# Kernel tuning notes

Hardware: AMD Instinct MI355X
Metric: run time of the kernel (lower is better)

Reference implementation:

```python
import jax, jax.numpy as jnp
import numpy as np


def _gather(feat, idx):
    # feat: [B, L, F], idx: [B, L, D] -> [B, L, D, F]  (per-molecule neighbor gather)
    return jax.vmap(lambda f, i: f[i])(feat, idx)


def setup_inputs() -> dict:
    key = jax.random.key(0)
    ks = jax.random.split(key, 16)
    B, L, D, F, FA, FB, R = 256, 128, 6, 200, 39, 10, 2
    s = 0.05
    return {
        "atom_list": jax.random.normal(ks[0], (B, L, FA), jnp.float32),
        "bond_list": jax.random.normal(ks[1], (B, L, FB), jnp.float32),
        "atom_degree": jax.random.randint(ks[2], (B, L, D), 0, L, jnp.int32),
        "bond_degree": jax.random.randint(ks[3], (B, L, D), 0, L, jnp.int32),
        "atom_W": jax.random.normal(ks[4], (F, FA), jnp.float32) * s,
        "atom_b": jax.random.normal(ks[5], (F,), jnp.float32) * s,
        "nbr_W": jax.random.normal(ks[6], (F, FA + FB), jnp.float32) * s,
        "nbr_b": jax.random.normal(ks[7], (F,), jnp.float32) * s,
        "align_W": jax.random.normal(ks[8], (R, 1, 2 * F), jnp.float32) * s,
        "align_b": jax.random.normal(ks[9], (R, 1), jnp.float32) * s,
        "attend_W": jax.random.normal(ks[10], (R, F, F), jnp.float32) * s,
        "attend_b": jax.random.normal(ks[11], (R, F), jnp.float32) * s,
        "gru_Wih": jax.random.normal(ks[12], (R, 3 * F, F), jnp.float32) * s,
        "gru_Whh": jax.random.normal(ks[13], (R, 3 * F, F), jnp.float32) * s,
        "gru_bih": jax.random.normal(ks[14], (R, 3 * F), jnp.float32) * s,
        "gru_bhh": jax.random.normal(ks[15], (R, 3 * F), jnp.float32) * s,
    }


def reference(atom_list, bond_list, atom_degree, bond_degree,
              atom_W, atom_b, nbr_W, nbr_b,
              align_W, align_b, attend_W, attend_b,
              gru_Wih, gru_Whh, gru_bih, gru_bhh):
    B, L, _ = atom_list.shape
    F = atom_W.shape[0]
    R = align_W.shape[0]
    pad = L - 1  # padding atom index convention from metaGAT

    # masks over padded neighbor slots: [B, L, D, 1]
    is_pad = (atom_degree == pad)[..., None]
    attend_mask = jnp.where(is_pad, 0.0, 1.0).astype(atom_list.dtype)
    softmax_mask = jnp.where(is_pad, -9e8, 0.0).astype(atom_list.dtype)

    # initial atom / neighbor embeddings
    atom_feat = jax.nn.leaky_relu(atom_list @ atom_W.T + atom_b)          # [B,L,F]
    atom_nbr = _gather(atom_list, atom_degree)                             # [B,L,D,FA]
    bond_nbr = _gather(bond_list, bond_degree)                             # [B,L,D,FB]
    nbr_feat = jax.nn.leaky_relu(
        jnp.concatenate([atom_nbr, bond_nbr], axis=-1) @ nbr_W.T + nbr_b)  # [B,L,D,F]

    cur = atom_feat  # GRU hidden / query features (activated after first step)
    for d in range(R):
        if d > 0:
            nbr_feat = _gather(cur, atom_degree)  # [B,L,D,F]
        cur_exp = jnp.broadcast_to(cur[:, :, None, :], nbr_feat.shape)
        feat_align = jnp.concatenate([cur_exp, nbr_feat], axis=-1)        # [B,L,D,2F]
        score = jax.nn.leaky_relu(feat_align @ align_W[d].T + align_b[d]) # [B,L,D,1]
        score = score + softmax_mask
        attn = jax.nn.softmax(score, axis=-2) * attend_mask               # [B,L,D,1]
        nbr_t = nbr_feat @ attend_W[d].T + attend_b[d]                    # [B,L,D,F]
        context = jax.nn.elu(jnp.sum(attn * nbr_t, axis=-2))              # [B,L,F]

        # GRUCell(input=context, hidden=cur)
        gi = context @ gru_Wih[d].T + gru_bih[d]                          # [B,L,3F]
        gh = cur @ gru_Whh[d].T + gru_bhh[d]                              # [B,L,3F]
        ir, iz, inn = jnp.split(gi, 3, axis=-1)
        hr, hz, hn = jnp.split(gh, 3, axis=-1)
        r = jax.nn.sigmoid(ir + hr)
        z = jax.nn.sigmoid(iz + hz)
        n = jnp.tanh(inn + r * hn)
        h = (1.0 - z) * n + z * cur
        cur = jax.nn.relu(h)  # activated_features for next step
    return cur
```

## Files before the change

### kernel.cpp

```cpp
#include <hip/hip_runtime.h>

#define B_     256
#define L_     128
#define D_     6
#define F_     200
#define FA_    39
#define FB_    10
#define PAD_   127
#define LMASK  127
#define NT     256
#define KC     (F_/4)
#define KC8    (F_/8)
#define NTILE  16
#define NQ     (NTILE * D_)
#define NF     (B_ * L_ * F_)
#define MSZ    (F_ * F_)
#define NNODES (B_ * L_)
#define NPAIRS (NNODES * D_)
#define KP     224
#define KPP    232
#define KSTEPS 7
#define NTL    13
#define FRAG_TOTAL (14 * NTL * KSTEPS * 64)

typedef __attribute__((ext_vector_type(8))) short sh8;
typedef __attribute__((ext_vector_type(4))) float f32x4;

__device__ __forceinline__ float lrelu(float x) { return x >= 0.0f ? x : 0.01f * x; }
__device__ __forceinline__ float sigm(float x)  { return 1.0f / (1.0f + __expf(-x)); }
__device__ __forceinline__ float fast_tanh(float x) {
    const float e = __expf(2.0f * x);
    return 1.0f - 2.0f / (e + 1.0f);
}
__device__ __forceinline__ unsigned short f2b(float x) {
    unsigned int u = __float_as_uint(x);
    unsigned int r = (u + 0x7FFFu + ((u >> 16) & 1u)) >> 16;
    return (unsigned short)r;
}
__device__ __forceinline__ float b2f(unsigned short u) {
    return __uint_as_float(((unsigned int)u) << 16);
}
#define AFRAG(arr, ks) (*(const sh8*)&arr[lane & 15][(ks) * 32 + ((lane >> 4) << 3)])
__device__ __forceinline__ sh8 bfrag(const unsigned short* __restrict__ WFr,
                                     int mat, int t, int ks, int lane) {
    return *(const sh8*)(WFr + ((((size_t)mat * NTL + t) * KSTEPS + ks) * 64 + lane) * 8);
}

#define PN2 32
__global__ __launch_bounds__(NT)
void prep_kernel(const float* __restrict__ atom_list, const float* __restrict__ bond_list,
                 const float* __restrict__ atom_W, const float* __restrict__ atom_b,
                 const float* __restrict__ nbr_W,
                 float* __restrict__ cur0, unsigned short* __restrict__ cur0b,
                 unsigned short* __restrict__ PA, unsigned short* __restrict__ PB)
{
    const int node0 = blockIdx.x * PN2;
    const int tid   = threadIdx.x;
    const int f     = tid;
    const bool valid = (f < F_);
    const int fc    = valid ? f : 0;

    __shared__ float wsh[F_ * (FA_ + FB_)];

    float wa[FA_];
    float wn[FA_ + FB_];

    for (int i = tid; i < F_ * FA_; i += NT) wsh[i] = atom_W[i];
    __syncthreads();
    #pragma unroll
    for (int k = 0; k < FA_; ++k) wa[k] = wsh[fc * FA_ + k];
    __syncthreads();
    for (int i = tid; i < F_ * (FA_ + FB_); i += NT) wsh[i] = nbr_W[i];
    __syncthreads();
    #pragma unroll
    for (int k = 0; k < FA_ + FB_; ++k) wn[k] = wsh[fc * (FA_ + FB_) + k];

    const float ab = atom_b[fc];

    for (int n = 0; n < PN2; ++n) {
        const float* __restrict__ ar = atom_list + (size_t)(node0 + n) * FA_;
        const float* __restrict__ br = bond_list + (size_t)(node0 + n) * FB_;
        float accA = ab, accPA = 0.0f, accPB = 0.0f;
        #pragma unroll
        for (int k = 0; k < FA_; ++k) {
            const float a = ar[k];
            accA  += a * wa[k];
            accPA += a * wn[k];
        }
        #pragma unroll
        for (int k = 0; k < FB_; ++k) accPB += br[k] * wn[FA_ + k];
        if (valid) {
            const size_t o = (size_t)(node0 + n) * F_ + f;
            const float c = lrelu(accA);
            cur0[o]  = c;
            cur0b[o] = f2b(c);
            PA[o]    = f2b(accPA);
            PB[o]    = f2b(accPB);
        }
    }
}

__global__ void build_frags(const float* __restrict__ attend_W,
                            const float* __restrict__ gru_Wih,
                            const float* __restrict__ gru_Whh,
                            unsigned short* __restrict__ WF)
{
    const int i = blockIdx.x * blockDim.x + threadIdx.x;
    if (i >= FRAG_TOTAL) return;
    const int lane = i & 63;
    int rest = i >> 6;
    const int ks = rest % KSTEPS; rest /= KSTEPS;
    const int t  = rest % NTL;
    const int m  = rest / NTL;
    const int n  = t * 16 + (lane & 15);
    const int k0 = ks * 32 + ((lane >> 4) << 3);
    const int r = m / 7, tt = m - r * 7;
    const float* src;
    if (tt == 0)      src = attend_W + (size_t)r * MSZ;
    else if (tt <= 3) src = gru_Wih + ((size_t)r * 3 + (tt - 1)) * MSZ;
    else              src = gru_Whh + ((size_t)r * 3 + (tt - 4)) * MSZ;
    unsigned short o[8];
    #pragma unroll
    for (int j = 0; j < 8; ++j) {
        const int k = k0 + j;
        const float v = (n < F_ && k < F_) ? src[(size_t)n * F_ + k] : 0.0f;
        o[j] = f2b(v);
    }
    uint4 w;
    w.x = (unsigned int)o[0] | ((unsigned int)o[1] << 16);
    w.y = (unsigned int)o[2] | ((unsigned int)o[3] << 16);
    w.z = (unsigned int)o[4] | ((unsigned int)o[5] << 16);
    w.w = (unsigned int)o[6] | ((unsigned int)o[7] << 16);
    ((uint4*)WF)[i] = w;
}

#define SN 32
__global__ __launch_bounds__(NT)
void score2_kernel(const float* __restrict__ feat, const float* __restrict__ alW2,
                   float* __restrict__ s2)
{
    const int tid  = threadIdx.x;
    const int node = blockIdx.x * SN + (tid >> 3);
    const int sub  = tid & 7;
    const float* row = feat + (size_t)node * F_;
    float b = 0.0f;
    for (int k = sub; k < F_; k += 8) b += row[k] * alW2[k];
    b += __shfl_xor(b, 1, 8); b += __shfl_xor(b, 2, 8); b += __shfl_xor(b, 4, 8);
    if (sub == 0) s2[node] = b;
}

#define PPB 32
__global__ __launch_bounds__(NT)
void pair_score_kernel(const int* __restrict__ atom_degree,
                       const int* __restrict__ bond_degree,
                       const unsigned short* __restrict__ PA,
                       const unsigned short* __restrict__ PB,
                       const float* __restrict__ alW2, const float* __restrict__ nbr_b,
                       float* __restrict__ s2p)
{
    __shared__ float w_s[F_], b_s[F_];
    const int tid = threadIdx.x;
    if (tid < F_) { w_s[tid] = alW2[tid]; b_s[tid] = nbr_b[tid]; }
    const int xcd = blockIdx.x & 7;
    const int j   = blockIdx.x >> 3;
    const int mol = (j / 24) * 8 + xcd;
    const int q0  = mol * (L_ * D_) + (j % 24) * PPB;
    const int q   = q0 + (tid >> 3);
    const int sub = tid & 7;
    const int nidx = atom_degree[q] & LMASK;
    const int bidx = bond_degree[q] & LMASK;
    const int bL   = mol * L_;
    const unsigned short* pa = PA + (size_t)(bL + nidx) * F_;
    const unsigned short* pb = PB + (size_t)(bL + bidx) * F_;
    __syncthreads();
    float s = 0.0f;
    for (int kk = sub; kk < KC8; kk += 8) {
        const sh8 pa8 = *(const sh8*)(pa + kk * 8);
        const sh8 pb8 = *(const sh8*)(pb + kk * 8);
        #pragma unroll
        for (int e = 0; e < 8; ++e)
            s += lrelu(b2f((unsigned short)pa8[e]) + b2f((unsigned short)pb8[e])
                       + b_s[kk * 8 + e]) * w_s[kk * 8 + e];
    }
    s += __shfl_xor(s, 1, 8); s += __shfl_xor(s, 2, 8); s += __shfl_xor(s, 4, 8);
    if (sub == 0) s2p[q] = s;
}

__global__ __launch_bounds__(NT, 4)
void round_kernel(
    const int*   __restrict__ atom_degree,
    const int*   __restrict__ bond_degree,
    const float* __restrict__ align_W,
    const float* __restrict__ align_b,
    const unsigned short* __restrict__ WF,
    const float* __restrict__ attend_b,
    const float* __restrict__ gru_bih,
    const float* __restrict__ gru_bhh,
    const float* __restrict__ nbr_b,
    const unsigned short* __restrict__ PAb,
    const unsigned short* __restrict__ PBb,
    const float* __restrict__ s2_tab,
    const float* __restrict__ cur_in,
    const unsigned short* __restrict__ cur_inb,
    float*       __restrict__ dst,
    unsigned short* __restrict__ dstb,
    int mode)
{
    const int bid   = blockIdx.x;
    const int mol   = ((bid >> 6) << 3) | (bid & 7);
    const int tile  = (bid >> 3) & 7;
    const int node0 = mol * L_ + tile * NTILE;
    const int bL    = mol * L_;
    const int tid   = threadIdx.x;
    const int lane  = tid & 63;
    const int wave  = tid >> 6;

    __shared__ __align__(16) unsigned short curb  [NTILE][KPP];
    __shared__ __align__(16) unsigned short mixedb[NTILE][KPP];
    __shared__ __align__(16) unsigned short ctxb  [NTILE][KPP];
    __shared__ __align__(16) float nbrb_s[F_];
    __shared__ float sc_s [NQ];
    __shared__ float asum_s[NTILE];
    __shared__ float s1_s[NTILE];
    __shared__ int   nidx_s[NQ];
    __shared__ int   bidx_s[NQ];

    for (int idx = tid; idx < NTILE * (KP - F_); idx += NT) {
        const int n = idx / (KP - F_), k = F_ + idx % (KP - F_);
        curb[n][k] = 0; mixedb[n][k] = 0; ctxb[n][k] = 0;
    }

    if (tid < NQ) {
        const int n = tid / D_, j = tid - n * D_;
        nidx_s[tid] = atom_degree[(node0 + n) * D_ + j] & LMASK;
        bidx_s[tid] = (mode == 0) ? (bond_degree[(node0 + n) * D_ + j] & LMASK) : 0;
    }
    if (mode == 0 && tid < F_) nbrb_s[tid] = nbr_b[tid];

    for (int idx = tid; idx < NTILE * KC8; idx += NT) {
        const int n = idx / KC8, kk = idx - n * KC8;
        *(uint4*)&curb[n][kk * 8] =
            *(const uint4*)(cur_inb + (size_t)(node0 + n) * F_ + kk * 8);
    }

    {
        const int n = tid >> 4, sub = tid & 15;
        const float* crow = cur_in + (size_t)(node0 + n) * F_;
        float a = 0.0f;
        for (int f = sub; f < F_; f += 16) a += crow[f] * align_W[f];
        a += __shfl_xor(a, 1, 16); a += __shfl_xor(a, 2, 16);
        a += __shfl_xor(a, 4, 16); a += __shfl_xor(a, 8, 16);
        if (sub == 0) s1_s[n] = a;
    }
    __syncthreads();

    if (tid < NQ) {
        const int n = tid / D_;
        const float s2v = (mode == 0)
            ? s2_tab[(size_t)(node0 + n) * D_ + (tid - n * D_)]
            : s2_tab[bL + nidx_s[tid]];
        float sc = lrelu(s1_s[n] + s2v + align_b[0]);
        if (nidx_s[tid] == PAD_) sc += -9.0e8f;
        sc_s[tid] = sc;
    }
    __syncthreads();

    if (tid < NTILE) {
        float m = sc_s[tid * D_];
        #pragma unroll
        for (int j = 1; j < D_; ++j) m = fmaxf(m, sc_s[tid * D_ + j]);
        float ex[D_]; float ssum = 0.0f;
        #pragma unroll
        for (int j = 0; j < D_; ++j) { ex[j] = __expf(sc_s[tid * D_ + j] - m); ssum += ex[j]; }
        const float inv = 1.0f / ssum;
        float as = 0.0f;
        #pragma unroll
        for (int j = 0; j < D_; ++j) {
            const float a = (nidx_s[tid * D_ + j] == PAD_) ? 0.0f : ex[j] * inv;
            sc_s[tid * D_ + j] = a;
            as += a;
        }
        asum_s[tid] = as;
    }
    __syncthreads();

    for (int idx = tid; idx < NTILE * KC8; idx += NT) {
        const int n = idx / KC8, kk = idx - n * KC8;
        const int c0 = kk * 8;
        float m[8];
        #pragma unroll
        for (int e = 0; e < 8; ++e) m[e] = 0.0f;
        if (mode == 0) {
            #pragma unroll
            for (int j = 0; j < D_; ++j) {
                const float a = sc_s[n * D_ + j];
                const sh8 pa8 = *(const sh8*)(PAb + (size_t)(bL + nidx_s[n*D_+j]) * F_ + c0);
                const sh8 pb8 = *(const sh8*)(PBb + (size_t)(bL + bidx_s[n*D_+j]) * F_ + c0);
                #pragma unroll
                for (int e = 0; e < 8; ++e)
                    m[e] += a * lrelu(b2f((unsigned short)pa8[e])
                                    + b2f((unsigned short)pb8[e]) + nbrb_s[c0 + e]);
            }
        } else {
            #pragma unroll
            for (int j = 0; j < D_; ++j) {
                const float a = sc_s[n * D_ + j];
                const sh8 v8 = *(const sh8*)(cur_inb + (size_t)(bL + nidx_s[n*D_+j]) * F_ + c0);
                #pragma unroll
                for (int e = 0; e < 8; ++e)
                    m[e] += a * b2f((unsigned short)v8[e]);
            }
        }
        uint4 w;
        w.x = (unsigned int)f2b(m[0]) | ((unsigned int)f2b(m[1]) << 16);
        w.y = (unsigned int)f2b(m[2]) | ((unsigned int)f2b(m[3]) << 16);
        w.z = (unsigned int)f2b(m[4]) | ((unsigned int)f2b(m[5]) << 16);
        w.w = (unsigned int)f2b(m[6]) | ((unsigned int)f2b(m[7]) << 16);
        *(uint4*)&mixedb[n][c0] = w;
    }
    __syncthreads();

    for (int t = wave; t < NTL; t += 4) {
        f32x4 acc = {0.f, 0.f, 0.f, 0.f};
        #pragma unroll
        for (int ks = 0; ks < KSTEPS; ++ks)
            acc = __builtin_amdgcn_mfma_f32_16x16x32_bf16(
                AFRAG(mixedb, ks), bfrag(WF, 0, t, ks, lane), acc, 0, 0, 0);
        const int f = t * 16 + (lane & 15);
        if (f < F_) {
            const float bb = attend_b[f];
            #pragma unroll
            for (int rg = 0; rg < 4; ++rg) {
                const int node = ((lane >> 4) << 2) + rg;
                float c = acc[rg] + asum_s[node] * bb;
                c = (c > 0.0f) ? c : (__expf(c) - 1.0f);
                ctxb[node][f] = f2b(c);
            }
        }
    }
    __syncthreads();

    for (int t = wave; t < NTL; t += 4) {
        f32x4 ar = {0.f,0.f,0.f,0.f}, az = {0.f,0.f,0.f,0.f};
        f32x4 ani = {0.f,0.f,0.f,0.f}, anh = {0.f,0.f,0.f,0.f};
        #pragma unroll
        for (int ks = 0; ks < KSTEPS; ++ks) {
            const sh8 ac = AFRAG(ctxb, ks);
            const sh8 ah = AFRAG(curb, ks);
            ar  = __builtin_amdgcn_mfma_f32_16x16x32_bf16(ac, bfrag(WF,1,t,ks,lane), ar, 0,0,0);
            ar  = __builtin_amdgcn_mfma_f32_16x16x32_bf16(ah, bfrag(WF,4,t,ks,lane), ar, 0,0,0);
            az  = __builtin_amdgcn_mfma_f32_16x16x32_bf16(ac, bfrag(WF,2,t,ks,lane), az, 0,0,0);
            az  = __builtin_amdgcn_mfma_f32_16x16x32_bf16(ah, bfrag(WF,5,t,ks,lane), az, 0,0,0);
            ani = __builtin_amdgcn_mfma_f32_16x16x32_bf16(ac, bfrag(WF,3,t,ks,lane), ani, 0,0,0);
            anh = __builtin_amdgcn_mfma_f32_16x16x32_bf16(ah, bfrag(WF,6,t,ks,lane), anh, 0,0,0);
        }
        const int f = t * 16 + (lane & 15);
        if (f < F_) {
            const float bir = gru_bih[f],        bhr = gru_bhh[f];
            const float biz = gru_bih[F_ + f],   bhz = gru_bhh[F_ + f];
            const float bin = gru_bih[2*F_ + f], bhn = gru_bhh[2*F_ + f];
            #pragma unroll
            for (int rg = 0; rg < 4; ++rg) {
                const int node = ((lane >> 4) << 2) + rg;
                const float r  = sigm(ar[rg] + bir + bhr);
                const float z  = sigm(az[rg] + biz + bhz);
                const float nn = fast_tanh(ani[rg] + bin + r * (anh[rg] + bhn));
                const size_t o = (size_t)(node0 + node) * F_ + f;
                const float cv = cur_in[o];
                const float h  = fmaxf((1.0f - z) * nn + z * cv, 0.0f);
                dst[o] = h;
                if (mode == 0) dstb[o] = f2b(h);
            }
        }
    }
}

extern "C" __attribute__((visibility("default")))
void kernel_launch(void* const* d_in, const int* in_sizes, int n_in,
                   void* d_out, int out_size, void* d_ws, size_t ws_size,
                   hipStream_t stream) {
    const float* atom_list = (const float*)d_in[0];
    const float* bond_list = (const float*)d_in[1];
    const int*   atom_deg  = (const int*)d_in[2];
    const int*   bond_deg  = (const int*)d_in[3];
    const float* atom_W    = (const float*)d_in[4];
    const float* atom_b    = (const float*)d_in[5];
    const float* nbr_W     = (const float*)d_in[6];
    const float* nbr_b     = (const float*)d_in[7];
    const float* align_W   = (const float*)d_in[8];
    const float* align_b   = (const float*)d_in[9];
    const float* attend_W  = (const float*)d_in[10];
    const float* attend_b  = (const float*)d_in[11];
    const float* gru_Wih   = (const float*)d_in[12];
    const float* gru_Whh   = (const float*)d_in[13];
    const float* gru_bih   = (const float*)d_in[14];
    const float* gru_bhh   = (const float*)d_in[15];

    float* ws   = (float*)d_ws;
    float* cur0 = ws;
    float* cur1 = ws + (size_t)NF;
    float* s2b  = ws + (size_t)2*NF;
    float* s2p  = s2b + NNODES;
    unsigned short* cur0b = (unsigned short*)(s2p + NPAIRS);
    unsigned short* cur1b = cur0b + (size_t)NF;
    unsigned short* PAb   = cur1b + (size_t)NF;
    unsigned short* PBb   = PAb   + (size_t)NF;
    unsigned short* WF    = PBb   + (size_t)NF;
    float* out  = (float*)d_out;

    prep_kernel<<<dim3(NNODES / PN2), dim3(NT), 0, stream>>>(
        atom_list, bond_list, atom_W, atom_b, nbr_W, cur0, cur0b, PAb, PBb);

    build_frags<<<dim3((FRAG_TOTAL + NT - 1) / NT), dim3(NT), 0, stream>>>(
        attend_W, gru_Wih, gru_Whh, WF);

    pair_score_kernel<<<dim3(NPAIRS / PPB), dim3(NT), 0, stream>>>(
        atom_deg, bond_deg, PAb, PBb, align_W + F_, nbr_b, s2p);

    const dim3 grid(NNODES / NTILE);
    const size_t rframe = (size_t)7 * NTL * KSTEPS * 64 * 8;

    round_kernel<<<grid, dim3(NT), 0, stream>>>(
        atom_deg, bond_deg, align_W, align_b,
        WF, attend_b, gru_bih, gru_bhh,
        nbr_b, PAb, PBb, s2p, cur0, cur0b, cur1, cur1b, 0);

    score2_kernel<<<dim3(NNODES / SN), dim3(NT), 0, stream>>>(
        cur1, align_W + 2 * F_ + F_, s2b);

    round_kernel<<<grid, dim3(NT), 0, stream>>>(
        atom_deg, bond_deg, align_W + 2 * F_, align_b + 1,
        WF + rframe, attend_b + F_, gru_bih + 3 * F_, gru_bhh + 3 * F_,
        nbr_b, PAb, PBb, s2b, cur1, cur1b, out, nullptr, 1);
}
```

Measured before the change: 356.3 us.

## Fuse frag build into prep and score2 into first round kernel epilogue

Merges the weight-fragment build into the prep kernel as extra blocks, removing one launch. It also computes the next round's per-node alignment score inside the round-0 GRU epilogue, using shuffle reductions plus LDS atomics, which removes the separate score2 kernel and its re-read of cur1. Separately, the neighbor gather loads are hoisted ahead of the accumulate loop so more loads are in flight. The cost is more register pressure in round_kernel and an extra barrier at the end of round 0.

After: 347.2 us. 2.5% less time.

```diff
diff --git a/kernel.cpp b/kernel.cpp
--- a/kernel.cpp
+++ b/kernel.cpp
@@ -22,6 +22,9 @@
 #define KSTEPS 7
 #define NTL    13
 #define FRAG_TOTAL (14 * NTL * KSTEPS * 64)
+#define PN2    32
+#define NPREP  (NNODES / PN2)
+#define NBF    ((FRAG_TOTAL + NT - 1) / NT)
 
 typedef __attribute__((ext_vector_type(8))) short sh8;
 typedef __attribute__((ext_vector_type(4))) float f32x4;
@@ -46,21 +49,55 @@
     return *(const sh8*)(WFr + ((((size_t)mat * NTL + t) * KSTEPS + ks) * 64 + lane) * 8);
 }
 
-#define PN2 32
 __global__ __launch_bounds__(NT)
-void prep_kernel(const float* __restrict__ atom_list, const float* __restrict__ bond_list,
-                 const float* __restrict__ atom_W, const float* __restrict__ atom_b,
-                 const float* __restrict__ nbr_W,
-                 float* __restrict__ cur0, unsigned short* __restrict__ cur0b,
-                 unsigned short* __restrict__ PA, unsigned short* __restrict__ PB)
+void prep_frags_kernel(const float* __restrict__ atom_list, const float* __restrict__ bond_list,
+                       const float* __restrict__ atom_W, const float* __restrict__ atom_b,
+                       const float* __restrict__ nbr_W,
+                       const float* __restrict__ attend_W,
+                       const float* __restrict__ gru_Wih,
+                       const float* __restrict__ gru_Whh,
+                       float* __restrict__ cur0, unsigned short* __restrict__ cur0b,
+                       unsigned short* __restrict__ PA, unsigned short* __restrict__ PB,
+                       unsigned short* __restrict__ WF)
 {
+    __shared__ float wsh[F_ * (FA_ + FB_)];
+    const int tid = threadIdx.x;
+
+    if (blockIdx.x >= NPREP) {
+        const int i = (blockIdx.x - NPREP) * NT + tid;
+        if (i >= FRAG_TOTAL) return;
+        const int lane = i & 63;
+        int rest = i >> 6;
+        const int ks = rest % KSTEPS; rest /= KSTEPS;
+        const int t  = rest % NTL;
+        const int m  = rest / NTL;
+        const int n  = t * 16 + (lane & 15);
+        const int k0 = ks * 32 + ((lane >> 4) << 3);
+        const int r = m / 7, tt = m - r * 7;
+        const float* src;
+        if (tt == 0)      src = attend_W + (size_t)r * MSZ;
+        else if (tt <= 3) src = gru_Wih + ((size_t)r * 3 + (tt - 1)) * MSZ;
+        else              src = gru_Whh + ((size_t)r * 3 + (tt - 4)) * MSZ;
+        unsigned short o[8];
+        #pragma unroll
+        for (int j = 0; j < 8; ++j) {
+            const int k = k0 + j;
+            const float v = (n < F_ && k < F_) ? src[(size_t)n * F_ + k] : 0.0f;
+            o[j] = f2b(v);
+        }
+        uint4 w;
+        w.x = (unsigned int)o[0] | ((unsigned int)o[1] << 16);
+        w.y = (unsigned int)o[2] | ((unsigned int)o[3] << 16);
+        w.z = (unsigned int)o[4] | ((unsigned int)o[5] << 16);
+        w.w = (unsigned int)o[6] | ((unsigned int)o[7] << 16);
+        ((uint4*)WF)[i] = w;
+        return;
+    }
+
     const int node0 = blockIdx.x * PN2;
-    const int tid   = threadIdx.x;
     const int f     = tid;
     const bool valid = (f < F_);
     const int fc    = valid ? f : 0;
-
-    __shared__ float wsh[F_ * (FA_ + FB_)];
 
     float wa[FA_];
     float wn[FA_ + FB_];
@@ -98,55 +135,6 @@
             PB[o]    = f2b(accPB);
         }
     }
-}
-
-__global__ void build_frags(const float* __restrict__ attend_W,
-                            const float* __restrict__ gru_Wih,
-                            const float* __restrict__ gru_Whh,
-                            unsigned short* __restrict__ WF)
-{
-    const int i = blockIdx.x * blockDim.x + threadIdx.x;
-    if (i >= FRAG_TOTAL) return;
-    const int lane = i & 63;
-    int rest = i >> 6;
-    const int ks = rest % KSTEPS; rest /= KSTEPS;
-    const int t  = rest % NTL;
-    const int m  = rest / NTL;
-    const int n  = t * 16 + (lane & 15);
-    const int k0 = ks * 32 + ((lane >> 4) << 3);
-    const int r = m / 7, tt = m - r * 7;
-    const float* src;
-    if (tt == 0)      src = attend_W + (size_t)r * MSZ;
-    else if (tt <= 3) src = gru_Wih + ((size_t)r * 3 + (tt - 1)) * MSZ;
-    else              src = gru_Whh + ((size_t)r * 3 + (tt - 4)) * MSZ;
-    unsigned short o[8];
-    #pragma unroll
-    for (int j = 0; j < 8; ++j) {
-        const int k = k0 + j;
-        const float v = (n < F_ && k < F_) ? src[(size_t)n * F_ + k] : 0.0f;
-        o[j] = f2b(v);
-    }
-    uint4 w;
-    w.x = (unsigned int)o[0] | ((unsigned int)o[1] << 16);
-    w.y = (unsigned int)o[2] | ((unsigned int)o[3] << 16);
-    w.z = (unsigned int)o[4] | ((unsigned int)o[5] << 16);
-    w.w = (unsigned int)o[6] | ((unsigned int)o[7] << 16);
-    ((uint4*)WF)[i] = w;
-}
-
-#define SN 32
-__global__ __launch_bounds__(NT)
-void score2_kernel(const float* __restrict__ feat, const float* __restrict__ alW2,
-                   float* __restrict__ s2)
-{
-    const int tid  = threadIdx.x;
-    const int node = blockIdx.x * SN + (tid >> 3);
-    const int sub  = tid & 7;
-    const float* row = feat + (size_t)node * F_;
-    float b = 0.0f;
-    for (int k = sub; k < F_; k += 8) b += row[k] * alW2[k];
-    b += __shfl_xor(b, 1, 8); b += __shfl_xor(b, 2, 8); b += __shfl_xor(b, 4, 8);
-    if (sub == 0) s2[node] = b;
 }
 
 #define PPB 32
@@ -204,6 +192,8 @@
     const unsigned short* __restrict__ cur_inb,
     float*       __restrict__ dst,
     unsigned short* __restrict__ dstb,
+    const float* __restrict__ alW2_next,
+    float*       __restrict__ s2_next,
     int mode)
 {
     const int bid   = blockIdx.x;
@@ -222,6 +212,7 @@
     __shared__ float sc_s [NQ];
     __shared__ float asum_s[NTILE];
     __shared__ float s1_s[NTILE];
+    __shared__ float s2acc[NTILE];
     __shared__ int   nidx_s[NQ];
     __shared__ int   bidx_s[NQ];
 
@@ -229,6 +220,7 @@
         const int n = idx / (KP - F_), k = F_ + idx % (KP - F_);
         curb[n][k] = 0; mixedb[n][k] = 0; ctxb[n][k] = 0;
     }
+    if (tid < NTILE) s2acc[tid] = 0.0f;
 
     if (tid < NQ) {
         const int n = tid / D_, j = tid - n * D_;
@@ -291,24 +283,31 @@
         #pragma unroll
         for (int e = 0; e < 8; ++e) m[e] = 0.0f;
         if (mode == 0) {
+            sh8 pa8[D_], pb8[D_];
+            #pragma unroll
+            for (int j = 0; j < D_; ++j) {
+                pa8[j] = *(const sh8*)(PAb + (size_t)(bL + nidx_s[n*D_+j]) * F_ + c0);
+                pb8[j] = *(const sh8*)(PBb + (size_t)(bL + bidx_s[n*D_+j]) * F_ + c0);
+            }
             #pragma unroll
             for (int j = 0; j < D_; ++j) {
                 const float a = sc_s[n * D_ + j];
-                const sh8 pa8 = *(const sh8*)(PAb + (size_t)(bL + nidx_s[n*D_+j]) * F_ + c0);
-                const sh8 pb8 = *(const sh8*)(PBb + (size_t)(bL + bidx_s[n*D_+j]) * F_ + c0);
                 #pragma unroll
                 for (int e = 0; e < 8; ++e)
-                    m[e] += a * lrelu(b2f((unsigned short)pa8[e])
-                                    + b2f((unsigned short)pb8[e]) + nbrb_s[c0 + e]);
+                    m[e] += a * lrelu(b2f((unsigned short)pa8[j][e])
+                                    + b2f((unsigned short)pb8[j][e]) + nbrb_s[c0 + e]);
             }
         } else {
+            sh8 v8[D_];
+            #pragma unroll
+            for (int j = 0; j < D_; ++j)
+                v8[j] = *(const sh8*)(cur_inb + (size_t)(bL + nidx_s[n*D_+j]) * F_ + c0);
             #pragma unroll
             for (int j = 0; j < D_; ++j) {
                 const float a = sc_s[n * D_ + j];
-                const sh8 v8 = *(const sh8*)(cur_inb + (size_t)(bL + nidx_s[n*D_+j]) * F_ + c0);
                 #pragma unroll
                 for (int e = 0; e < 8; ++e)
-                    m[e] += a * b2f((unsigned short)v8[e]);
+                    m[e] += a * b2f((unsigned short)v8[j][e]);
             }
         }
         uint4 w;
@@ -340,6 +339,7 @@
     }
     __syncthreads();
 
+    float s2part[4] = {0.f, 0.f, 0.f, 0.f};
     for (int t = wave; t < NTL; t += 4) {
         f32x4 ar = {0.f,0.f,0.f,0.f}, az = {0.f,0.f,0.f,0.f};
         f32x4 ani = {0.f,0.f,0.f,0.f}, anh = {0.f,0.f,0.f,0.f};
@@ -359,6 +359,7 @@
             const float bir = gru_bih[f],        bhr = gru_bhh[f];
             const float biz = gru_bih[F_ + f],   bhz = gru_bhh[F_ + f];
             const float bin = gru_bih[2*F_ + f], bhn = gru_bhh[2*F_ + f];
+            const float w2 = (mode == 0) ? alW2_next[f] : 0.0f;
             #pragma unroll
             for (int rg = 0; rg < 4; ++rg) {
                 const int node = ((lane >> 4) << 2) + rg;
@@ -369,9 +370,21 @@
                 const float cv = cur_in[o];
                 const float h  = fmaxf((1.0f - z) * nn + z * cv, 0.0f);
                 dst[o] = h;
-                if (mode == 0) dstb[o] = f2b(h);
+                if (mode == 0) { dstb[o] = f2b(h); s2part[rg] += h * w2; }
             }
         }
+    }
+
+    if (mode == 0) {
+        #pragma unroll
+        for (int rg = 0; rg < 4; ++rg) {
+            float v = s2part[rg];
+            v += __shfl_xor(v, 1, 16); v += __shfl_xor(v, 2, 16);
+            v += __shfl_xor(v, 4, 16); v += __shfl_xor(v, 8, 16);
+            if ((lane & 15) == 0) atomicAdd(&s2acc[((lane >> 4) << 2) + rg], v);
+        }
+        __syncthreads();
+        if (tid < NTILE) s2_next[node0 + tid] = s2acc[tid];
     }
 }
 
@@ -408,11 +421,10 @@
     unsigned short* WF    = PBb   + (size_t)NF;
     float* out  = (float*)d_out;
 
-    prep_kernel<<<dim3(NNODES / PN2), dim3(NT), 0, stream>>>(
-        atom_list, bond_list, atom_W, atom_b, nbr_W, cur0, cur0b, PAb, PBb);
-
-    build_frags<<<dim3((FRAG_TOTAL + NT - 1) / NT), dim3(NT), 0, stream>>>(
-        attend_W, gru_Wih, gru_Whh, WF);
+    prep_frags_kernel<<<dim3(NPREP + NBF), dim3(NT), 0, stream>>>(
+        atom_list, bond_list, atom_W, atom_b, nbr_W,
+        attend_W, gru_Wih, gru_Whh,
+        cur0, cur0b, PAb, PBb, WF);
 
     pair_score_kernel<<<dim3(NPAIRS / PPB), dim3(NT), 0, stream>>>(
         atom_deg, bond_deg, PAb, PBb, align_W + F_, nbr_b, s2p);
@@ -423,13 +435,12 @@
     round_kernel<<<grid, dim3(NT), 0, stream>>>(
         atom_deg, bond_deg, align_W, align_b,
         WF, attend_b, gru_bih, gru_bhh,
-        nbr_b, PAb, PBb, s2p, cur0, cur0b, cur1, cur1b, 0);
-
-    score2_kernel<<<dim3(NNODES / SN), dim3(NT), 0, stream>>>(
-        cur1, align_W + 2 * F_ + F_, s2b);
+        nbr_b, PAb, PBb, s2p, cur0, cur0b, cur1, cur1b,
+        align_W + 2 * F_ + F_, s2b, 0);
 
     round_kernel<<<grid, dim3(NT), 0, stream>>>(
         atom_deg, bond_deg, align_W + 2 * F_, align_b + 1,
         WF + rframe, attend_b + F_, gru_bih + 3 * F_, gru_bhh + 3 * F_,
-        nbr_b, PAb, PBb, s2b, cur1, cur1b, out, nullptr, 1);
-}
+        nbr_b, PAb, PBb, s2b, cur1, cur1b, out, nullptr,
+        nullptr, nullptr, 1);
+}
```
